# Kernel optimization log

Measured on AMD Instinct MI355X. Metric: run time of the kernel, lower is better.

The kernel has to match this reference:

```python
import jax, jax.numpy as jnp
import numpy as np

N_LAYERS = 6
N_HEADS = 16
D_MODEL = 1024
D_HEAD = D_MODEL // N_HEADS
D_FF = 4096
VOCAB = 32000
MAX_LEN = 1024
B, T = 2, 1024
NEG = -1e9
EPS = 1e-5


def layernorm(x, s, b):
    mu = jnp.mean(x, axis=-1, keepdims=True)
    var = jnp.mean(jnp.square(x - mu), axis=-1, keepdims=True)
    return (x - mu) * jax.lax.rsqrt(var + EPS) * s + b


def setup_inputs() -> dict:
    key = jax.random.key(0)
    ks = jax.random.split(key, 8)
    s = 0.02
    return {
        "idx": jax.random.randint(ks[0], (B, T), 0, VOCAB),
        "tok_emb": jax.random.normal(ks[1], (VOCAB, D_MODEL), jnp.float32) * s,
        "pos_emb": jax.random.normal(ks[2], (MAX_LEN, D_MODEL), jnp.float32) * s,
        "ln1_s": jnp.ones((N_LAYERS, D_MODEL), jnp.float32),
        "ln1_b": jnp.zeros((N_LAYERS, D_MODEL), jnp.float32),
        "qkv_w": jax.random.normal(ks[3], (N_LAYERS, D_MODEL, 3 * D_MODEL), jnp.float32) * s,
        "qkv_b": jnp.zeros((N_LAYERS, 3 * D_MODEL), jnp.float32),
        "out_w": jax.random.normal(ks[4], (N_LAYERS, D_MODEL, D_MODEL), jnp.float32) * s,
        "out_b": jnp.zeros((N_LAYERS, D_MODEL), jnp.float32),
        "ln2_s": jnp.ones((N_LAYERS, D_MODEL), jnp.float32),
        "ln2_b": jnp.zeros((N_LAYERS, D_MODEL), jnp.float32),
        "mlp_w1": jax.random.normal(ks[5], (N_LAYERS, D_MODEL, D_FF), jnp.float32) * s,
        "mlp_b1": jnp.zeros((N_LAYERS, D_FF), jnp.float32),
        "mlp_w2": jax.random.normal(ks[6], (N_LAYERS, D_FF, D_MODEL), jnp.float32) * s,
        "mlp_b2": jnp.zeros((N_LAYERS, D_MODEL), jnp.float32),
        "lnf_s": jnp.ones((D_MODEL,), jnp.float32),
        "lnf_b": jnp.zeros((D_MODEL,), jnp.float32),
        "head_w": jax.random.normal(ks[7], (D_MODEL, VOCAB), jnp.float32) * s,
    }


def reference(idx, tok_emb, pos_emb, ln1_s, ln1_b, qkv_w, qkv_b, out_w, out_b,
              ln2_s, ln2_b, mlp_w1, mlp_b1, mlp_w2, mlp_b2, lnf_s, lnf_b, head_w):
    b, t = idx.shape
    x = tok_emb[idx] + pos_emb[:t]  # [B,T,D]
    causal = jnp.tril(jnp.ones((t, t), dtype=bool))
    scale = 1.0 / np.sqrt(D_HEAD)
    for l in range(N_LAYERS):
        h = layernorm(x, ln1_s[l], ln1_b[l])
        qkv = h @ qkv_w[l] + qkv_b[l]  # [B,T,3D]
        q, k, v = jnp.split(qkv, 3, axis=-1)
        q = q.reshape(b, t, N_HEADS, D_HEAD).transpose(0, 2, 1, 3)
        k = k.reshape(b, t, N_HEADS, D_HEAD).transpose(0, 2, 1, 3)
        v = v.reshape(b, t, N_HEADS, D_HEAD).transpose(0, 2, 1, 3)
        att = jnp.einsum('bhqd,bhkd->bhqk', q, k) * scale
        att = jnp.where(causal, att, NEG)
        att = jax.nn.softmax(att, axis=-1)
        y = jnp.einsum('bhqk,bhkd->bhqd', att, v)
        y = y.transpose(0, 2, 1, 3).reshape(b, t, D_MODEL)
        x = x + (y @ out_w[l] + out_b[l])
        h = layernorm(x, ln2_s[l], ln2_b[l])
        m = jax.nn.gelu(h @ mlp_w1[l] + mlp_b1[l], approximate=False) @ mlp_w2[l] + mlp_b2[l]
        x = x + m
    x = layernorm(x, lnf_s, lnf_b)
    logits = x @ head_w  # [B,T,V]
    return logits
```

## Files before the change

kernel.cpp:

```cpp
#include <hip/hip_runtime.h>


#define T_SEQ 1024
#define NTOK  2048
#define DM    1024
#define DFF   4096
#define NH    16
#define DH    64
#define NL    6
#define VOCAB 32000

typedef short sx8 __attribute__((ext_vector_type(8)));
typedef float fx4 __attribute__((ext_vector_type(4)));
typedef unsigned short usx4 __attribute__((ext_vector_type(4)));
typedef unsigned int   uix4 __attribute__((ext_vector_type(4)));

__device__ __forceinline__ unsigned short f2bf(float f) {
  union { float f; unsigned u; } c; c.f = f;
  unsigned r = c.u + 0x7FFFu + ((c.u >> 16) & 1u);
  return (unsigned short)(r >> 16);
}
__device__ __forceinline__ float bf2f(unsigned short u) {
  union { unsigned u; float f; } c; c.u = ((unsigned)u) << 16;
  return c.f;
}

__device__ __forceinline__ void gload_lds16(const unsigned short* g, unsigned short* l) {
  __builtin_amdgcn_global_load_lds(
      (const __attribute__((address_space(1))) unsigned int*)g,
      (__attribute__((address_space(3))) unsigned int*)l, 16, 0, 0);
}

__device__ __forceinline__ int xcd_swizzle(int orig, int nwg) {
  int q = nwg >> 3, r = nwg & 7;
  int xcd = orig & 7, idx = orig >> 3;
  int base = (xcd < r) ? xcd * (q + 1) : r * (q + 1) + (xcd - r) * q;
  return base + idx;
}

__global__ __launch_bounds__(256) void k_embed(const int* __restrict__ idx,
                                               const float* __restrict__ tok,
                                               const float* __restrict__ pos,
                                               float* __restrict__ x) {
  int token = blockIdx.x;
  int t = token & (T_SEQ - 1);
  int id = idx[token];
  int c = threadIdx.x * 4;
  float4 tv = *(const float4*)&tok[(size_t)id * DM + c];
  float4 pv = *(const float4*)&pos[(size_t)t * DM + c];
  float4 r;
  r.x = tv.x + pv.x; r.y = tv.y + pv.y; r.z = tv.z + pv.z; r.w = tv.w + pv.w;
  *(float4*)&x[(size_t)token * DM + c] = r;
}

__global__ __launch_bounds__(256) void k_ln(const float* __restrict__ x,
                                            const float* __restrict__ g,
                                            const float* __restrict__ b,
                                            unsigned short* __restrict__ h) {
  int row = blockIdx.x;
  int tid = threadIdx.x;
  float4 v = *(const float4*)&x[(size_t)row * DM + tid * 4];
  float s = v.x + v.y + v.z + v.w;
  float q = v.x * v.x + v.y * v.y + v.z * v.z + v.w * v.w;
  for (int off = 32; off > 0; off >>= 1) {
    s += __shfl_down(s, off);
    q += __shfl_down(q, off);
  }
  __shared__ float red[8];
  int wid = tid >> 6, lane = tid & 63;
  if (lane == 0) { red[wid] = s; red[4 + wid] = q; }
  __syncthreads();
  s = red[0] + red[1] + red[2] + red[3];
  q = red[4] + red[5] + red[6] + red[7];
  float mu = s * (1.0f / DM);
  float var = q * (1.0f / DM) - mu * mu;
  float rstd = rsqrtf(var + 1e-5f);
  float4 gg = *(const float4*)&g[tid * 4];
  float4 bb = *(const float4*)&b[tid * 4];
  usx4 o;
  o[0] = f2bf((v.x - mu) * rstd * gg.x + bb.x);
  o[1] = f2bf((v.y - mu) * rstd * gg.y + bb.y);
  o[2] = f2bf((v.z - mu) * rstd * gg.z + bb.z);
  o[3] = f2bf((v.w - mu) * rstd * gg.w + bb.w);
  *(usx4*)&h[(size_t)row * DM + tid * 4] = o;
}

__global__ __launch_bounds__(256) void k_reduce_ln(const unsigned short* __restrict__ part,
                                                   float* __restrict__ x,
                                                   const float* __restrict__ g,
                                                   const float* __restrict__ b,
                                                   unsigned short* __restrict__ h) {
  int row = blockIdx.x;
  int tid = threadIdx.x;
  int c = tid * 4;
  float4 v = *(const float4*)&x[(size_t)row * DM + c];
#pragma unroll
  for (int s4 = 0; s4 < 2; ++s4) {
    usx4 p = *(const usx4*)&part[((size_t)s4 * NTOK + row) * DM + c];
    v.x += bf2f(p[0]); v.y += bf2f(p[1]); v.z += bf2f(p[2]); v.w += bf2f(p[3]);
  }
  *(float4*)&x[(size_t)row * DM + c] = v;
  float s = v.x + v.y + v.z + v.w;
  float q = v.x * v.x + v.y * v.y + v.z * v.z + v.w * v.w;
  for (int off = 32; off > 0; off >>= 1) {
    s += __shfl_down(s, off);
    q += __shfl_down(q, off);
  }
  __shared__ float red[8];
  int wid = tid >> 6, lane = tid & 63;
  if (lane == 0) { red[wid] = s; red[4 + wid] = q; }
  __syncthreads();
  s = red[0] + red[1] + red[2] + red[3];
  q = red[4] + red[5] + red[6] + red[7];
  float mu = s * (1.0f / DM);
  float var = q * (1.0f / DM) - mu * mu;
  float rstd = rsqrtf(var + 1e-5f);
  float4 gg = *(const float4*)&g[c];
  float4 bb = *(const float4*)&b[c];
  usx4 o;
  o[0] = f2bf((v.x - mu) * rstd * gg.x + bb.x);
  o[1] = f2bf((v.y - mu) * rstd * gg.y + bb.y);
  o[2] = f2bf((v.z - mu) * rstd * gg.z + bb.z);
  o[3] = f2bf((v.w - mu) * rstd * gg.w + bb.w);
  *(usx4*)&h[(size_t)row * DM + c] = o;
}

__global__ __launch_bounds__(256) void k_wtrans(const float* __restrict__ W,
                                                unsigned short* __restrict__ WT,
                                                int K, int N) {
  __shared__ float t[64][68];
  int k0 = blockIdx.x * 64, n0 = blockIdx.y * 64;
  int tid = threadIdx.x;
#pragma unroll
  for (int i = 0; i < 4; ++i) {
    int chunk = i * 256 + tid;
    int r = chunk >> 4, c = (chunk & 15) << 2;
    float4 v = *(const float4*)&W[(size_t)(k0 + r) * N + n0 + c];
    t[r][c] = v.x; t[r][c + 1] = v.y; t[r][c + 2] = v.z; t[r][c + 3] = v.w;
  }
  __syncthreads();
#pragma unroll
  for (int i = 0; i < 4; ++i) {
    int chunk = i * 256 + tid;
    int n = chunk >> 4, c = (chunk & 15) << 2;
    usx4 o;
    o[0] = f2bf(t[c][n]);
    o[1] = f2bf(t[c + 1][n]);
    o[2] = f2bf(t[c + 2][n]);
    o[3] = f2bf(t[c + 3][n]);
    *(usx4*)&WT[(size_t)(n0 + n) * K + k0 + c] = o;
  }
}

template <int EPI>
__global__ __launch_bounds__(256) void k_gemm(const unsigned short* __restrict__ A,
                                              const unsigned short* __restrict__ BT,
                                              const float* __restrict__ bias,
                                              unsigned short* __restrict__ part,
                                              unsigned short* __restrict__ outb,
                                              float* __restrict__ outf,
                                              int N, int K, int NT, int KS) {
  __shared__ unsigned short As[128 * 64];
  __shared__ unsigned short Bs[128 * 64];
  int tid = threadIdx.x;
  int wid = tid >> 6, lane = tid & 63;
  int lr = lane & 15, lg = lane >> 4;

  int id = xcd_swizzle(blockIdx.x, gridDim.x);
  int mt = id & 15;
  int rest = id >> 4;
  int nt = rest % NT;
  int ks = rest / NT;
  int m0 = mt * 128, n0 = nt * 128;
  int Kslice = K / KS;
  int kbeg = ks * Kslice, kend = kbeg + Kslice;

  int wm = (wid >> 1) * 64, wn = (wid & 1) * 64;

  fx4 acc[4][4] = {};

  for (int kt = kbeg; kt < kend; kt += 64) {
    __syncthreads();
#pragma unroll
    for (int i = 0; i < 4; ++i) {
      int chunk = i * 256 + tid;
      int r = chunk >> 3;
      int slot = chunk & 7;
      int c = ((slot ^ (r & 7)) << 3);
      gload_lds16(&A[(size_t)(m0 + r) * K + kt + c], &As[chunk << 3]);
      gload_lds16(&BT[(size_t)(n0 + r) * K + kt + c], &Bs[chunk << 3]);
    }
    __syncthreads();
#pragma unroll
    for (int kk = 0; kk < 2; ++kk) {
      int slotz = (kk * 4 + lg) ^ (lr & 7);
      sx8 fa[4], fb[4];
#pragma unroll
      for (int mi = 0; mi < 4; ++mi)
        fa[mi] = *(const sx8*)&As[(wm + mi * 16 + lr) * 64 + slotz * 8];
#pragma unroll
      for (int ni = 0; ni < 4; ++ni)
        fb[ni] = *(const sx8*)&Bs[(wn + ni * 16 + lr) * 64 + slotz * 8];
#pragma unroll
      for (int mi = 0; mi < 4; ++mi)
#pragma unroll
        for (int ni = 0; ni < 4; ++ni)
          acc[mi][ni] = __builtin_amdgcn_mfma_f32_16x16x32_bf16(fb[ni], fa[mi], acc[mi][ni], 0, 0, 0);
    }
  }

#pragma unroll
  for (int ni = 0; ni < 4; ++ni) {
    int col0 = n0 + wn + ni * 16 + lg * 4;
    float4 bv = {0.f, 0.f, 0.f, 0.f};
    if (bias && ks == 0) bv = *(const float4*)&bias[col0];
#pragma unroll
    for (int mi = 0; mi < 4; ++mi) {
      int row = m0 + wm + mi * 16 + lr;
      float v0 = acc[mi][ni][0] + bv.x;
      float v1 = acc[mi][ni][1] + bv.y;
      float v2 = acc[mi][ni][2] + bv.z;
      float v3 = acc[mi][ni][3] + bv.w;
      if constexpr (EPI == 0) {
        int bb = row >> 10, tt = row & 1023;
        if (col0 < 2048) {
          int which = col0 >> 10;
          int hc = col0 & 1023;
          usx4 o = {f2bf(v0), f2bf(v1), f2bf(v2), f2bf(v3)};
          *(usx4*)&outb[(size_t)which * NTOK * DM +
                        (((size_t)bb * NH + (hc >> 6)) * T_SEQ + tt) * DH + (hc & 63)] = o;
        } else {
          int dc = col0 - 2048;
          unsigned short* vt = outb + (size_t)2 * NTOK * DM;
          size_t base = (((size_t)bb * NH + (dc >> 6)) * DH + (dc & 63)) * T_SEQ + tt;
          vt[base] = f2bf(v0);
          vt[base + T_SEQ] = f2bf(v1);
          vt[base + 2 * T_SEQ] = f2bf(v2);
          vt[base + 3 * T_SEQ] = f2bf(v3);
        }
      } else if constexpr (EPI == 1) {
        usx4 o;
        o[0] = f2bf(0.5f * v0 * (1.0f + erff(v0 * 0.70710678f)));
        o[1] = f2bf(0.5f * v1 * (1.0f + erff(v1 * 0.70710678f)));
        o[2] = f2bf(0.5f * v2 * (1.0f + erff(v2 * 0.70710678f)));
        o[3] = f2bf(0.5f * v3 * (1.0f + erff(v3 * 0.70710678f)));
        *(usx4*)&outb[(size_t)row * N + col0] = o;
      } else {
        usx4 o = {f2bf(v0), f2bf(v1), f2bf(v2), f2bf(v3)};
        *(usx4*)&part[((size_t)ks * NTOK + row) * DM + col0] = o;
      }
    }
  }
}

#define LDSUB(buf, ab, kk) (lds + (((buf) * 2 + (ab)) * 2 + (kk)) * 8192)

__device__ __forceinline__ void stage_half(const unsigned short* g, int rowstride,
                                           unsigned short* ldsbase, int tid, int k0) {
#pragma unroll
  for (int r = 0; r < 2; ++r) {
    int chunk = r * 512 + tid;
    int row = chunk >> 2, slot = chunk & 3;
    gload_lds16(g + (size_t)row * rowstride + k0 + ((slot ^ ((row >> 1) & 3)) << 3),
                ldsbase + (chunk << 3));
  }
}

__global__ __launch_bounds__(512, 2) void k_gemm256(const unsigned short* __restrict__ A,
                                                    const unsigned short* __restrict__ BT,
                                                    float* __restrict__ outf,
                                                    int N, int K) {
  __shared__ unsigned short lds[8 * 8192];
  int tid = threadIdx.x;
  int wid = tid >> 6, lane = tid & 63;
  int lr = lane & 15, lg = lane >> 4;
  int wm2 = wid >> 2, wn4 = wid & 3;
  int id = xcd_swizzle(blockIdx.x, gridDim.x);
  int mt = id & 7, nt = id >> 3;
  int m0 = mt * 256, n0 = nt * 256;
  const unsigned short* Ab = A + (size_t)m0 * K;
  const unsigned short* Bb = BT + (size_t)n0 * K;
  int NIT = K >> 7;
  int swz = (lg ^ ((lr >> 1) & 3)) << 3;
  float* obase = outf + (size_t)(m0 + wm2 * 128 + lr) * N + n0 + wn4 * 64 + lg * 4;

  fx4 acc[8][4] = {};

  stage_half(Ab, K, LDSUB(0, 0, 0), tid, 0);
  stage_half(Bb, K, LDSUB(0, 1, 0), tid, 0);
  stage_half(Ab, K, LDSUB(0, 0, 1), tid, 32);
  stage_half(Bb, K, LDSUB(0, 1, 1), tid, 32);
  stage_half(Ab, K, LDSUB(1, 0, 0), tid, 64);
  stage_half(Bb, K, LDSUB(1, 1, 0), tid, 64);
  stage_half(Ab, K, LDSUB(1, 0, 1), tid, 96);
  asm volatile("s_waitcnt vmcnt(6)" ::: "memory");
  __builtin_amdgcn_s_barrier();

#define PHASE(BUF, KK, NHH, LOADA, STG, VMW)                                         \
  {                                                                                  \
    if (LOADA) {                                                                     \
      const unsigned short* sA = LDSUB(BUF, 0, KK);                                  \
      _Pragma("unroll")                                                              \
      for (int mi = 0; mi < 8; ++mi)                                                 \
        fa[mi] = *(const sx8*)&sA[(wm2 * 128 + mi * 16 + lr) * 32 + swz];            \
    }                                                                                \
    {                                                                                \
      const unsigned short* sB = LDSUB(BUF, 1, KK);                                  \
      _Pragma("unroll")                                                              \
      for (int j = 0; j < 2; ++j)                                                    \
        fb[j] = *(const sx8*)&sB[(wn4 * 64 + (NHH) * 32 + j * 16 + lr) * 32 + swz];  \
    }                                                                                \
    STG;                                                                             \
    VMW;                                                                             \
    __builtin_amdgcn_sched_barrier(0);                                               \
    __builtin_amdgcn_s_barrier();                                                    \
    asm volatile("s_waitcnt lgkmcnt(0)" ::: "memory");                               \
    __builtin_amdgcn_sched_barrier(0);                                               \
    __builtin_amdgcn_s_setprio(1);                                                   \
    _Pragma("unroll")                                                                \
    for (int mi = 0; mi < 8; ++mi) {                                                 \
      acc[mi][(NHH) * 2 + 0] = __builtin_amdgcn_mfma_f32_16x16x32_bf16(              \
          fb[0], fa[mi], acc[mi][(NHH) * 2 + 0], 0, 0, 0);                           \
      acc[mi][(NHH) * 2 + 1] = __builtin_amdgcn_mfma_f32_16x16x32_bf16(              \
          fb[1], fa[mi], acc[mi][(NHH) * 2 + 1], 0, 0, 0);                           \
    }                                                                                \
    __builtin_amdgcn_s_setprio(0);                                                   \
    __builtin_amdgcn_sched_barrier(0);                                               \
    __builtin_amdgcn_s_barrier();                                                    \
  }

  for (int it = 0; it < NIT; ++it) {
    bool st = (it < NIT - 1);
    bool last = (it == NIT - 1);
    int t1k = (2 * it + 1) * 64;
    int t2k = (2 * it + 2) * 64;
    int t3k = (2 * it + 3) * 64;
    sx8 fa[8], fb[2];

    PHASE(0, 0, 0, true,
          { stage_half(Bb, K, LDSUB(1, 1, 1), tid, t1k + 32); }, {});
    PHASE(0, 0, 1, false,
          { if (st) stage_half(Ab, K, LDSUB(0, 0, 0), tid, t2k); }, {});
    PHASE(0, 1, 0, true,
          { if (st) stage_half(Bb, K, LDSUB(0, 1, 0), tid, t2k); }, {});
    PHASE(0, 1, 1, false,
          { if (st) stage_half(Ab, K, LDSUB(0, 0, 1), tid, t2k + 32); },
          { if (last) { asm volatile("s_waitcnt vmcnt(0)" ::: "memory"); }
            else      { asm volatile("s_waitcnt vmcnt(6)" ::: "memory"); } });
    PHASE(1, 0, 0, true,
          { if (st) stage_half(Bb, K, LDSUB(0, 1, 1), tid, t2k + 32); }, {});
    PHASE(1, 0, 1, false,
          { if (st) stage_half(Ab, K, LDSUB(1, 0, 0), tid, t3k); }, {});
    PHASE(1, 1, 0, true,
          { if (st) stage_half(Bb, K, LDSUB(1, 1, 0), tid, t3k); }, {});
    if (last) {
#pragma unroll
      for (int mi = 0; mi < 8; ++mi) {
        *(float4*)(obase + (size_t)mi * 16 * N) =
            (float4){acc[mi][0][0], acc[mi][0][1], acc[mi][0][2], acc[mi][0][3]};
        *(float4*)(obase + (size_t)mi * 16 * N + 16) =
            (float4){acc[mi][1][0], acc[mi][1][1], acc[mi][1][2], acc[mi][1][3]};
      }
    }
    PHASE(1, 1, 1, false,
          { if (st) stage_half(Ab, K, LDSUB(1, 0, 1), tid, t3k + 32); },
          { if (!last) { asm volatile("s_waitcnt vmcnt(6)" ::: "memory"); } });
  }
#undef PHASE

#pragma unroll
  for (int mi = 0; mi < 8; ++mi) {
    *(float4*)(obase + (size_t)mi * 16 * N + 32) =
        (float4){acc[mi][2][0], acc[mi][2][1], acc[mi][2][2], acc[mi][2][3]};
    *(float4*)(obase + (size_t)mi * 16 * N + 48) =
        (float4){acc[mi][3][0], acc[mi][3][1], acc[mi][3][2], acc[mi][3][3]};
  }
}

__global__ __launch_bounds__(256) void k_attn(const unsigned short* __restrict__ gq,
                                              const unsigned short* __restrict__ gk,
                                              const unsigned short* __restrict__ gvt,
                                              unsigned short* __restrict__ y) {
  __shared__ unsigned short Ks[128 * 64];
  __shared__ unsigned short Vt[64 * 128];
  __shared__ unsigned short Pw[4][16 * 136];
  int id = xcd_swizzle(blockIdx.x, gridDim.x);
  int bh = id >> 3, pr = id & 7;
  int tid = threadIdx.x, wid = tid >> 6, lane = tid & 63;
  int lr = lane & 15, lg = lane >> 4;
  const float SCL = 0.125f * 1.44269504f;

  for (int half = 0; half < 2; ++half) {
    int qt = half ? (15 - pr) : pr;
    int q0 = qt * 64 + wid * 16;
    int qg = q0 + lr;

    sx8 qf[2];
    {
      const unsigned short* qp = gq + ((size_t)bh * T_SEQ + qg) * DH + lg * 8;
      qf[0] = *(const sx8*)qp;
      qf[1] = *(const sx8*)(qp + 32);
    }

    fx4 yacc[4] = {};
    float mrun = -1e30f, lrun = 0.f;

    int jmax = qt >> 1;
    for (int j = 0; j <= jmax; ++j) {
      int kt0 = j * 128;
      __syncthreads();
#pragma unroll
      for (int i = 0; i < 4; ++i) {
        int chunk = i * 256 + tid;
        {
          int r = chunk >> 3, s = chunk & 7;
          gload_lds16(&gk[((size_t)bh * T_SEQ + kt0 + r) * DH + ((s ^ (r & 7)) << 3)],
                      &Ks[chunk << 3]);
        }
        {
          int r = chunk >> 4, s = chunk & 15;
          gload_lds16(&gvt[((size_t)bh * DH + r) * T_SEQ + kt0 + ((s ^ (r & 15)) << 3)],
                      &Vt[chunk << 3]);
        }
      }
      __syncthreads();

      fx4 st[8] = {};
#pragma unroll
      for (int kk = 0; kk < 2; ++kk) {
        int slotz = (kk * 4 + lg) ^ (lr & 7);
#pragma unroll
        for (int mi = 0; mi < 8; ++mi) {
          sx8 kb = *(const sx8*)&Ks[(mi * 16 + lr) * 64 + slotz * 8];
          st[mi] = __builtin_amdgcn_mfma_f32_16x16x32_bf16(kb, qf[kk], st[mi], 0, 0, 0);
        }
      }

      float pvv[8][4];
      float pmax = -1e30f;
      bool lastj = (j == jmax);
#pragma unroll
      for (int mi = 0; mi < 8; ++mi)
#pragma unroll
        for (int rg = 0; rg < 4; ++rg) {
          float val = st[mi][rg] * SCL;
          if (lastj && (kt0 + mi * 16 + lg * 4 + rg) > qg) val = -1e30f;
          pvv[mi][rg] = val;
          pmax = fmaxf(pmax, val);
        }
      pmax = fmaxf(pmax, __shfl_xor(pmax, 16));
      pmax = fmaxf(pmax, __shfl_xor(pmax, 32));
      if (!__all(pmax <= mrun + 11.5f)) {
        float mnew = fmaxf(mrun, pmax);
        float sc = exp2f(mrun - mnew);
        lrun *= sc;
#pragma unroll
        for (int dt = 0; dt < 4; ++dt)
#pragma unroll
          for (int rg = 0; rg < 4; ++rg) yacc[dt][rg] *= sc;
        mrun = mnew;
      }
      float ps = 0.f;
#pragma unroll
      for (int mi = 0; mi < 8; ++mi)
#pragma unroll
        for (int rg = 0; rg < 4; ++rg) {
          float e = exp2f(pvv[mi][rg] - mrun);
          pvv[mi][rg] = e;
          ps += e;
        }
      ps += __shfl_xor(ps, 16);
      ps += __shfl_xor(ps, 32);
      lrun += ps;

#pragma unroll
      for (int mi = 0; mi < 8; ++mi)
#pragma unroll
        for (int rp = 0; rp < 2; ++rp) {
          unsigned pk = (unsigned)f2bf(pvv[mi][rp * 2]) |
                        ((unsigned)f2bf(pvv[mi][rp * 2 + 1]) << 16);
          *(unsigned*)&Pw[wid][lr * 136 + mi * 16 + lg * 4 + rp * 2] = pk;
        }

#pragma unroll
      for (int kk = 0; kk < 4; ++kk) {
        sx8 pa = *(const sx8*)&Pw[wid][lr * 136 + kk * 32 + lg * 8];
        int slotz = (kk * 4 + lg) ^ lr;
#pragma unroll
        for (int dt = 0; dt < 4; ++dt) {
          sx8 vb = *(const sx8*)&Vt[(dt * 16 + lr) * 128 + slotz * 8];
          yacc[dt] = __builtin_amdgcn_mfma_f32_16x16x32_bf16(vb, pa, yacc[dt], 0, 0, 0);
        }
      }
    }

    float inv = 1.0f / lrun;
    int tok = (bh >> 4) * T_SEQ + qg;
    int colbase = (bh & 15) * DH;
#pragma unroll
    for (int dt = 0; dt < 4; ++dt) {
      usx4 o;
#pragma unroll
      for (int rg = 0; rg < 4; ++rg) o[rg] = f2bf(yacc[dt][rg] * inv);
      *(usx4*)&y[(size_t)tok * DM + colbase + dt * 16 + lg * 4] = o;
    }
  }
}

extern "C" void kernel_launch(void* const* d_in, const int* in_sizes, int n_in,
                              void* d_out, int out_size, void* d_ws, size_t ws_size,
                              hipStream_t stream) {
  (void)in_sizes; (void)n_in; (void)out_size; (void)ws_size;
  const int*   idx     = (const int*)d_in[0];
  const float* tok_emb = (const float*)d_in[1];
  const float* pos_emb = (const float*)d_in[2];
  const float* ln1_s   = (const float*)d_in[3];
  const float* ln1_b   = (const float*)d_in[4];
  const float* qkv_w   = (const float*)d_in[5];
  const float* qkv_b   = (const float*)d_in[6];
  const float* out_w   = (const float*)d_in[7];
  const float* out_b   = (const float*)d_in[8];
  const float* ln2_s   = (const float*)d_in[9];
  const float* ln2_b   = (const float*)d_in[10];
  const float* mlp_w1  = (const float*)d_in[11];
  const float* mlp_b1  = (const float*)d_in[12];
  const float* mlp_w2  = (const float*)d_in[13];
  const float* mlp_b2  = (const float*)d_in[14];
  const float* lnf_s   = (const float*)d_in[15];
  const float* lnf_b   = (const float*)d_in[16];
  const float* head_w  = (const float*)d_in[17];

  char* p = (char*)d_ws;
  float* x          = (float*)p;          p += (size_t)NTOK * DM * 4;
  unsigned short* h = (unsigned short*)p; p += (size_t)NTOK * DM * 2;
  unsigned short* qkvb = (unsigned short*)p; p += (size_t)3 * NTOK * DM * 2;
  unsigned short* yb = (unsigned short*)p; p += (size_t)NTOK * DM * 2;
  unsigned short* m1 = (unsigned short*)p; p += (size_t)NTOK * DFF * 2;
  unsigned short* wt = (unsigned short*)p;
  unsigned short* part = (unsigned short*)(p + 32 * 1024 * 1024);

  dim3 blk(256);

  k_embed<<<NTOK, blk, 0, stream>>>(idx, tok_emb, pos_emb, x);
  k_ln<<<NTOK, blk, 0, stream>>>(x, ln1_s, ln1_b, h);

  for (int l = 0; l < NL; ++l) {
    k_wtrans<<<dim3(DM / 64, 3 * DM / 64), blk, 0, stream>>>(qkv_w + (size_t)l * DM * 3 * DM, wt, DM, 3 * DM);
    k_gemm<0><<<16 * 24, blk, 0, stream>>>(h, wt, qkv_b + l * 3 * DM,
                                           nullptr, qkvb, nullptr, 3 * DM, DM, 24, 1);
    k_attn<<<256, blk, 0, stream>>>(qkvb, qkvb + (size_t)NTOK * DM,
                                    qkvb + (size_t)2 * NTOK * DM, yb);
    k_wtrans<<<dim3(DM / 64, DM / 64), blk, 0, stream>>>(out_w + (size_t)l * DM * DM, wt, DM, DM);
    k_gemm<2><<<16 * 8 * 2, blk, 0, stream>>>(yb, wt, out_b + l * DM,
                                              part, nullptr, nullptr, DM, DM, 8, 2);
    k_reduce_ln<<<NTOK, blk, 0, stream>>>(part, x, ln2_s + l * DM, ln2_b + l * DM, h);
    k_wtrans<<<dim3(DM / 64, DFF / 64), blk, 0, stream>>>(mlp_w1 + (size_t)l * DM * DFF, wt, DM, DFF);
    k_gemm<1><<<16 * 32, blk, 0, stream>>>(h, wt, mlp_b1 + l * DFF,
                                           nullptr, m1, nullptr, DFF, DM, 32, 1);
    k_wtrans<<<dim3(DFF / 64, DM / 64), blk, 0, stream>>>(mlp_w2 + (size_t)l * DFF * DM, wt, DFF, DM);
    k_gemm<2><<<16 * 8 * 2, blk, 0, stream>>>(m1, wt, mlp_b2 + l * DM,
                                              part, nullptr, nullptr, DM, DFF, 8, 2);
    if (l < NL - 1)
      k_reduce_ln<<<NTOK, blk, 0, stream>>>(part, x, ln1_s + (l + 1) * DM, ln1_b + (l + 1) * DM, h);
    else
      k_reduce_ln<<<NTOK, blk, 0, stream>>>(part, x, lnf_s, lnf_b, h);
  }

  k_wtrans<<<dim3(DM / 64, VOCAB / 64), blk, 0, stream>>>(head_w, wt, DM, VOCAB);
  k_gemm256<<<1000, 512, 0, stream>>>(h, wt, (float*)d_out, VOCAB, DM);
}
```

Measured before the change: 1.230 ms.

## Double-buffer GEMM LDS loads, split attention per q-tile, raise split-K to four

The generic GEMM gets two LDS buffers so the next K tile's global-to-LDS loads are issued while MFMAs run on the current tile, with explicit waitcnt and barriers in place of the old per-tile load-then-sync. The attention kernel now launches one block per (batch-head, q-tile) instead of pairing tiles inside each block, which doubles the grid to raise occupancy. The out-projection and MLP-down GEMMs move from split-K 2 to 4 to fill more CUs, and the reduce-LN kernel now sums four partials. The costs are doubled GEMM LDS use, extra partial-buffer traffic, and a less even causal-attention workload per block.

Measured after the change: 1.160 ms. 1.06x faster.

```diff
diff --git a/kernel.cpp b/kernel.cpp
--- a/kernel.cpp
+++ b/kernel.cpp
@@ -95,7 +95,7 @@
   int c = tid * 4;
   float4 v = *(const float4*)&x[(size_t)row * DM + c];
 #pragma unroll
-  for (int s4 = 0; s4 < 2; ++s4) {
+  for (int s4 = 0; s4 < 4; ++s4) {
     usx4 p = *(const usx4*)&part[((size_t)s4 * NTOK + row) * DM + c];
     v.x += bf2f(p[0]); v.y += bf2f(p[1]); v.z += bf2f(p[2]); v.w += bf2f(p[3]);
   }
@@ -160,8 +160,8 @@
                                               unsigned short* __restrict__ outb,
                                               float* __restrict__ outf,
                                               int N, int K, int NT, int KS) {
-  __shared__ unsigned short As[128 * 64];
-  __shared__ unsigned short Bs[128 * 64];
+  __shared__ unsigned short As[2][128 * 64];
+  __shared__ unsigned short Bs[2][128 * 64];
   int tid = threadIdx.x;
   int wid = tid >> 6, lane = tid & 63;
   int lr = lane & 15, lg = lane >> 4;
@@ -173,41 +173,58 @@
   int ks = rest / NT;
   int m0 = mt * 128, n0 = nt * 128;
   int Kslice = K / KS;
-  int kbeg = ks * Kslice, kend = kbeg + Kslice;
+  int kbeg = ks * Kslice;
+  int nk = Kslice >> 6;
 
   int wm = (wid >> 1) * 64, wn = (wid & 1) * 64;
 
   fx4 acc[4][4] = {};
 
-  for (int kt = kbeg; kt < kend; kt += 64) {
-    __syncthreads();
-#pragma unroll
-    for (int i = 0; i < 4; ++i) {
-      int chunk = i * 256 + tid;
-      int r = chunk >> 3;
-      int slot = chunk & 7;
-      int c = ((slot ^ (r & 7)) << 3);
-      gload_lds16(&A[(size_t)(m0 + r) * K + kt + c], &As[chunk << 3]);
-      gload_lds16(&BT[(size_t)(n0 + r) * K + kt + c], &Bs[chunk << 3]);
-    }
-    __syncthreads();
+#define GSTAGE(buf, kt)                                                         \
+  {                                                                             \
+    _Pragma("unroll")                                                           \
+    for (int i = 0; i < 4; ++i) {                                               \
+      int chunk = i * 256 + tid;                                                \
+      int r = chunk >> 3, slot = chunk & 7;                                     \
+      int c = ((slot ^ (r & 7)) << 3);                                          \
+      gload_lds16(&A[(size_t)(m0 + r) * K + (kt) + c], &As[buf][chunk << 3]);   \
+      gload_lds16(&BT[(size_t)(n0 + r) * K + (kt) + c], &Bs[buf][chunk << 3]);  \
+    }                                                                           \
+  }
+
+  GSTAGE(0, kbeg);
+  for (int ik = 0; ik < nk; ++ik) {
+    int cur = ik & 1;
+    if (ik + 1 < nk) {
+      GSTAGE(cur ^ 1, kbeg + (ik + 1) * 64);
+      asm volatile("s_waitcnt vmcnt(8)" ::: "memory");
+    } else {
+      asm volatile("s_waitcnt vmcnt(0)" ::: "memory");
+    }
+    __builtin_amdgcn_sched_barrier(0);
+    __builtin_amdgcn_s_barrier();
+    __builtin_amdgcn_sched_barrier(0);
 #pragma unroll
     for (int kk = 0; kk < 2; ++kk) {
       int slotz = (kk * 4 + lg) ^ (lr & 7);
       sx8 fa[4], fb[4];
 #pragma unroll
       for (int mi = 0; mi < 4; ++mi)
-        fa[mi] = *(const sx8*)&As[(wm + mi * 16 + lr) * 64 + slotz * 8];
+        fa[mi] = *(const sx8*)&As[cur][(wm + mi * 16 + lr) * 64 + slotz * 8];
 #pragma unroll
       for (int ni = 0; ni < 4; ++ni)
-        fb[ni] = *(const sx8*)&Bs[(wn + ni * 16 + lr) * 64 + slotz * 8];
+        fb[ni] = *(const sx8*)&Bs[cur][(wn + ni * 16 + lr) * 64 + slotz * 8];
 #pragma unroll
       for (int mi = 0; mi < 4; ++mi)
 #pragma unroll
         for (int ni = 0; ni < 4; ++ni)
           acc[mi][ni] = __builtin_amdgcn_mfma_f32_16x16x32_bf16(fb[ni], fa[mi], acc[mi][ni], 0, 0, 0);
     }
-  }
+    asm volatile("s_waitcnt lgkmcnt(0)" ::: "memory");
+    __builtin_amdgcn_sched_barrier(0);
+    __builtin_amdgcn_s_barrier();
+  }
+#undef GSTAGE
 
 #pragma unroll
   for (int ni = 0; ni < 4; ++ni) {
@@ -385,125 +402,121 @@
   __shared__ unsigned short Vt[64 * 128];
   __shared__ unsigned short Pw[4][16 * 136];
   int id = xcd_swizzle(blockIdx.x, gridDim.x);
-  int bh = id >> 3, pr = id & 7;
+  int bh = id >> 4, qt = 15 - (id & 15);
   int tid = threadIdx.x, wid = tid >> 6, lane = tid & 63;
   int lr = lane & 15, lg = lane >> 4;
+  int q0 = qt * 64 + wid * 16;
+  int qg = q0 + lr;
   const float SCL = 0.125f * 1.44269504f;
 
-  for (int half = 0; half < 2; ++half) {
-    int qt = half ? (15 - pr) : pr;
-    int q0 = qt * 64 + wid * 16;
-    int qg = q0 + lr;
-
-    sx8 qf[2];
-    {
-      const unsigned short* qp = gq + ((size_t)bh * T_SEQ + qg) * DH + lg * 8;
-      qf[0] = *(const sx8*)qp;
-      qf[1] = *(const sx8*)(qp + 32);
-    }
-
-    fx4 yacc[4] = {};
-    float mrun = -1e30f, lrun = 0.f;
-
-    int jmax = qt >> 1;
-    for (int j = 0; j <= jmax; ++j) {
-      int kt0 = j * 128;
-      __syncthreads();
-#pragma unroll
-      for (int i = 0; i < 4; ++i) {
-        int chunk = i * 256 + tid;
-        {
-          int r = chunk >> 3, s = chunk & 7;
-          gload_lds16(&gk[((size_t)bh * T_SEQ + kt0 + r) * DH + ((s ^ (r & 7)) << 3)],
-                      &Ks[chunk << 3]);
-        }
-        {
-          int r = chunk >> 4, s = chunk & 15;
-          gload_lds16(&gvt[((size_t)bh * DH + r) * T_SEQ + kt0 + ((s ^ (r & 15)) << 3)],
-                      &Vt[chunk << 3]);
-        }
-      }
-      __syncthreads();
-
-      fx4 st[8] = {};
-#pragma unroll
-      for (int kk = 0; kk < 2; ++kk) {
-        int slotz = (kk * 4 + lg) ^ (lr & 7);
-#pragma unroll
-        for (int mi = 0; mi < 8; ++mi) {
-          sx8 kb = *(const sx8*)&Ks[(mi * 16 + lr) * 64 + slotz * 8];
-          st[mi] = __builtin_amdgcn_mfma_f32_16x16x32_bf16(kb, qf[kk], st[mi], 0, 0, 0);
-        }
-      }
-
-      float pvv[8][4];
-      float pmax = -1e30f;
-      bool lastj = (j == jmax);
-#pragma unroll
-      for (int mi = 0; mi < 8; ++mi)
-#pragma unroll
-        for (int rg = 0; rg < 4; ++rg) {
-          float val = st[mi][rg] * SCL;
-          if (lastj && (kt0 + mi * 16 + lg * 4 + rg) > qg) val = -1e30f;
-          pvv[mi][rg] = val;
-          pmax = fmaxf(pmax, val);
-        }
-      pmax = fmaxf(pmax, __shfl_xor(pmax, 16));
-      pmax = fmaxf(pmax, __shfl_xor(pmax, 32));
-      if (!__all(pmax <= mrun + 11.5f)) {
-        float mnew = fmaxf(mrun, pmax);
-        float sc = exp2f(mrun - mnew);
-        lrun *= sc;
-#pragma unroll
-        for (int dt = 0; dt < 4; ++dt)
-#pragma unroll
-          for (int rg = 0; rg < 4; ++rg) yacc[dt][rg] *= sc;
-        mrun = mnew;
-      }
-      float ps = 0.f;
-#pragma unroll
-      for (int mi = 0; mi < 8; ++mi)
-#pragma unroll
-        for (int rg = 0; rg < 4; ++rg) {
-          float e = exp2f(pvv[mi][rg] - mrun);
-          pvv[mi][rg] = e;
-          ps += e;
-        }
-      ps += __shfl_xor(ps, 16);
-      ps += __shfl_xor(ps, 32);
-      lrun += ps;
-
-#pragma unroll
-      for (int mi = 0; mi < 8; ++mi)
-#pragma unroll
-        for (int rp = 0; rp < 2; ++rp) {
-          unsigned pk = (unsigned)f2bf(pvv[mi][rp * 2]) |
-                        ((unsigned)f2bf(pvv[mi][rp * 2 + 1]) << 16);
-          *(unsigned*)&Pw[wid][lr * 136 + mi * 16 + lg * 4 + rp * 2] = pk;
-        }
-
-#pragma unroll
-      for (int kk = 0; kk < 4; ++kk) {
-        sx8 pa = *(const sx8*)&Pw[wid][lr * 136 + kk * 32 + lg * 8];
-        int slotz = (kk * 4 + lg) ^ lr;
-#pragma unroll
-        for (int dt = 0; dt < 4; ++dt) {
-          sx8 vb = *(const sx8*)&Vt[(dt * 16 + lr) * 128 + slotz * 8];
-          yacc[dt] = __builtin_amdgcn_mfma_f32_16x16x32_bf16(vb, pa, yacc[dt], 0, 0, 0);
-        }
-      }
-    }
-
-    float inv = 1.0f / lrun;
-    int tok = (bh >> 4) * T_SEQ + qg;
-    int colbase = (bh & 15) * DH;
-#pragma unroll
-    for (int dt = 0; dt < 4; ++dt) {
-      usx4 o;
-#pragma unroll
-      for (int rg = 0; rg < 4; ++rg) o[rg] = f2bf(yacc[dt][rg] * inv);
-      *(usx4*)&y[(size_t)tok * DM + colbase + dt * 16 + lg * 4] = o;
-    }
+  sx8 qf[2];
+  {
+    const unsigned short* qp = gq + ((size_t)bh * T_SEQ + qg) * DH + lg * 8;
+    qf[0] = *(const sx8*)qp;
+    qf[1] = *(const sx8*)(qp + 32);
+  }
+
+  fx4 yacc[4] = {};
+  float mrun = -1e30f, lrun = 0.f;
+
+  int jmax = qt >> 1;
+  for (int j = 0; j <= jmax; ++j) {
+    int kt0 = j * 128;
+    __syncthreads();
+#pragma unroll
+    for (int i = 0; i < 4; ++i) {
+      int chunk = i * 256 + tid;
+      {
+        int r = chunk >> 3, s = chunk & 7;
+        gload_lds16(&gk[((size_t)bh * T_SEQ + kt0 + r) * DH + ((s ^ (r & 7)) << 3)],
+                    &Ks[chunk << 3]);
+      }
+      {
+        int r = chunk >> 4, s = chunk & 15;
+        gload_lds16(&gvt[((size_t)bh * DH + r) * T_SEQ + kt0 + ((s ^ (r & 15)) << 3)],
+                    &Vt[chunk << 3]);
+      }
+    }
+    __syncthreads();
+
+    fx4 st[8] = {};
+#pragma unroll
+    for (int kk = 0; kk < 2; ++kk) {
+      int slotz = (kk * 4 + lg) ^ (lr & 7);
+#pragma unroll
+      for (int mi = 0; mi < 8; ++mi) {
+        sx8 kb = *(const sx8*)&Ks[(mi * 16 + lr) * 64 + slotz * 8];
+        st[mi] = __builtin_amdgcn_mfma_f32_16x16x32_bf16(kb, qf[kk], st[mi], 0, 0, 0);
+      }
+    }
+
+    float pvv[8][4];
+    float pmax = -1e30f;
+    bool lastj = (j == jmax);
+#pragma unroll
+    for (int mi = 0; mi < 8; ++mi)
+#pragma unroll
+      for (int rg = 0; rg < 4; ++rg) {
+        float val = st[mi][rg] * SCL;
+        if (lastj && (kt0 + mi * 16 + lg * 4 + rg) > qg) val = -1e30f;
+        pvv[mi][rg] = val;
+        pmax = fmaxf(pmax, val);
+      }
+    pmax = fmaxf(pmax, __shfl_xor(pmax, 16));
+    pmax = fmaxf(pmax, __shfl_xor(pmax, 32));
+    if (!__all(pmax <= mrun + 11.5f)) {
+      float mnew = fmaxf(mrun, pmax);
+      float sc = exp2f(mrun - mnew);
+      lrun *= sc;
+#pragma unroll
+      for (int dt = 0; dt < 4; ++dt)
+#pragma unroll
+        for (int rg = 0; rg < 4; ++rg) yacc[dt][rg] *= sc;
+      mrun = mnew;
+    }
+    float ps = 0.f;
+#pragma unroll
+    for (int mi = 0; mi < 8; ++mi)
+#pragma unroll
+      for (int rg = 0; rg < 4; ++rg) {
+        float e = exp2f(pvv[mi][rg] - mrun);
+        pvv[mi][rg] = e;
+        ps += e;
+      }
+    ps += __shfl_xor(ps, 16);
+    ps += __shfl_xor(ps, 32);
+    lrun += ps;
+
+#pragma unroll
+    for (int mi = 0; mi < 8; ++mi)
+#pragma unroll
+      for (int rp = 0; rp < 2; ++rp) {
+        unsigned pk = (unsigned)f2bf(pvv[mi][rp * 2]) |
+                      ((unsigned)f2bf(pvv[mi][rp * 2 + 1]) << 16);
+        *(unsigned*)&Pw[wid][lr * 136 + mi * 16 + lg * 4 + rp * 2] = pk;
+      }
+
+#pragma unroll
+    for (int kk = 0; kk < 4; ++kk) {
+      sx8 pa = *(const sx8*)&Pw[wid][lr * 136 + kk * 32 + lg * 8];
+      int slotz = (kk * 4 + lg) ^ lr;
+#pragma unroll
+      for (int dt = 0; dt < 4; ++dt) {
+        sx8 vb = *(const sx8*)&Vt[(dt * 16 + lr) * 128 + slotz * 8];
+        yacc[dt] = __builtin_amdgcn_mfma_f32_16x16x32_bf16(vb, pa, yacc[dt], 0, 0, 0);
+      }
+    }
+  }
+
+  float inv = 1.0f / lrun;
+  int tok = (bh >> 4) * T_SEQ + qg;
+  int colbase = (bh & 15) * DH;
+#pragma unroll
+  for (int dt = 0; dt < 4; ++dt) {
+    usx4 o;
+#pragma unroll
+    for (int rg = 0; rg < 4; ++rg) o[rg] = f2bf(yacc[dt][rg] * inv);
+    *(usx4*)&y[(size_t)tok * DM + colbase + dt * 16 + lg * 4] = o;
   }
 }
 
@@ -548,18 +561,18 @@
     k_wtrans<<<dim3(DM / 64, 3 * DM / 64), blk, 0, stream>>>(qkv_w + (size_t)l * DM * 3 * DM, wt, DM, 3 * DM);
     k_gemm<0><<<16 * 24, blk, 0, stream>>>(h, wt, qkv_b + l * 3 * DM,
                                            nullptr, qkvb, nullptr, 3 * DM, DM, 24, 1);
-    k_attn<<<256, blk, 0, stream>>>(qkvb, qkvb + (size_t)NTOK * DM,
+    k_attn<<<512, blk, 0, stream>>>(qkvb, qkvb + (size_t)NTOK * DM,
                                     qkvb + (size_t)2 * NTOK * DM, yb);
     k_wtrans<<<dim3(DM / 64, DM / 64), blk, 0, stream>>>(out_w + (size_t)l * DM * DM, wt, DM, DM);
-    k_gemm<2><<<16 * 8 * 2, blk, 0, stream>>>(yb, wt, out_b + l * DM,
-                                              part, nullptr, nullptr, DM, DM, 8, 2);
+    k_gemm<2><<<16 * 8 * 4, blk, 0, stream>>>(yb, wt, out_b + l * DM,
+                                              part, nullptr, nullptr, DM, DM, 8, 4);
     k_reduce_ln<<<NTOK, blk, 0, stream>>>(part, x, ln2_s + l * DM, ln2_b + l * DM, h);
     k_wtrans<<<dim3(DM / 64, DFF / 64), blk, 0, stream>>>(mlp_w1 + (size_t)l * DM * DFF, wt, DM, DFF);
     k_gemm<1><<<16 * 32, blk, 0, stream>>>(h, wt, mlp_b1 + l * DFF,
                                            nullptr, m1, nullptr, DFF, DM, 32, 1);
     k_wtrans<<<dim3(DFF / 64, DM / 64), blk, 0, stream>>>(mlp_w2 + (size_t)l * DFF * DM, wt, DFF, DM);
-    k_gemm<2><<<16 * 8 * 2, blk, 0, stream>>>(m1, wt, mlp_b2 + l * DM,
-                                              part, nullptr, nullptr, DM, DFF, 8, 2);
+    k_gemm<2><<<16 * 8 * 4, blk, 0, stream>>>(m1, wt, mlp_b2 + l * DM,
+                                              part, nullptr, nullptr, DM, DFF, 8, 4);
     if (l < NL - 1)
       k_reduce_ln<<<NTOK, blk, 0, stream>>>(part, x, ln1_s + (l + 1) * DM, ln1_b + (l + 1) * DM, h);
     else
```
